# Optimization experiments

Measured on AMD Instinct MI355X. Metric: run time of the kernel, lower is better.

## Reference

```python
import jax, jax.numpy as jnp
import numpy as np

N_HEADS = 16


def setup_inputs() -> dict:
    key = jax.random.key(0)
    ks = jax.random.split(key, 9)
    B, S, D = 2, 2048, 1024
    sc = 0.02
    return {
        'x': jax.random.normal(ks[0], (B, S, D), jnp.float32),
        'Wq': jax.random.normal(ks[1], (D, D), jnp.float32) * sc,
        'bq': jax.random.normal(ks[2], (D,), jnp.float32) * sc,
        'Wk': jax.random.normal(ks[3], (D, D), jnp.float32) * sc,
        'bk': jax.random.normal(ks[4], (D,), jnp.float32) * sc,
        'Wv': jax.random.normal(ks[5], (D, D), jnp.float32) * sc,
        'bv': jax.random.normal(ks[6], (D,), jnp.float32) * sc,
        'Wo': jax.random.normal(ks[7], (D, D), jnp.float32) * sc,
        'bo': jax.random.normal(ks[8], (D,), jnp.float32) * sc,
    }


def reference(x, Wq, bq, Wk, bk, Wv, bv, Wo, bo):
    # Chunked causal prefill. The chunk-wise mask (q_pos >= kv_pos over the
    # growing KV cache) is mathematically identical to full causal attention,
    # so we compute it as one vectorized masked softmax attention.
    B, S, D = x.shape
    H = N_HEADS
    hd = D // H

    def proj(W, b):
        # torch Linear: y = x @ W.T + b ; then split heads -> [B,H,S,hd]
        y = jnp.einsum('bsd,ed->bse', x, W) + b
        return y.reshape(B, S, H, hd).transpose(0, 2, 1, 3)

    q = proj(Wq, bq)
    k = proj(Wk, bk)
    v = proj(Wv, bv)

    scores = jnp.einsum('bhqd,bhkd->bhqk', q, k) / jnp.sqrt(jnp.asarray(hd, x.dtype))
    causal = jnp.tril(jnp.ones((S, S), dtype=bool))  # [S,S]
    scores = jnp.where(causal[None, None], scores, jnp.asarray(-jnp.inf, scores.dtype))
    attn = jax.nn.softmax(scores, axis=-1)
    ctx = jnp.einsum('bhqk,bhkd->bhqd', attn, v)  # [B,H,S,hd]
    ctx = ctx.transpose(0, 2, 1, 3).reshape(B, S, D)
    out = jnp.einsum('bsd,ed->bse', ctx, Wo) + bo
    return out
```

## Files before the change

### kernel.cpp

```cpp
#include <hip/hip_runtime.h>
#include <cstdint>
#include <math.h>

typedef _Float16 f16;
typedef _Float16 f16x2 __attribute__((ext_vector_type(2)));
typedef _Float16 f16x4 __attribute__((ext_vector_type(4)));
typedef _Float16 f16x8 __attribute__((ext_vector_type(8)));
typedef __fp16   h16x2 __attribute__((ext_vector_type(2)));
typedef float    f32x4 __attribute__((ext_vector_type(4)));

__device__ __forceinline__ f32x4 mfma16(f16x8 a, f16x8 b, f32x4 c) {
  return __builtin_amdgcn_mfma_f32_16x16x32_f16(a, b, c, 0, 0, 0);
}
__device__ __forceinline__ void gl2lds16(const f16* g, f16* l) {
  __builtin_amdgcn_global_load_lds((__attribute__((address_space(1))) void*)(g),
                                   (__attribute__((address_space(3))) void*)(l),
                                   16, 0, 0);
}
__device__ __forceinline__ float fexp2(float x) { return __builtin_amdgcn_exp2f(x); }
__device__ __forceinline__ f16x2 pkrtz(float a, float b) {
  h16x2 r = __builtin_amdgcn_cvt_pkrtz(a, b);
  return __builtin_bit_cast(f16x2, r);
}
__device__ __forceinline__ float dot2acc(f16x2 a, f16x2 b, float c) {
#if __has_builtin(__builtin_amdgcn_fdot2)
  return __builtin_amdgcn_fdot2(__builtin_bit_cast(h16x2, a),
                                __builtin_bit_cast(h16x2, b), c, false);
#else
  return c + (float)a[0] * (float)b[0] + (float)a[1] * (float)b[1];
#endif
}

__global__ __launch_bounds__(256) void cvt_kernel(
    const float* __restrict__ x,  const float* __restrict__ wq, const float* __restrict__ wk,
    const float* __restrict__ wv, const float* __restrict__ wo,
    f16* __restrict__ xh, f16* __restrict__ wqkvh, f16* __restrict__ woh)
{
  const int seg = blockIdx.y;
  const float* src; f16* dst; int n;
  if      (seg == 0) { src = x;  dst = xh;              n = 4194304; }
  else if (seg == 1) { src = wq; dst = wqkvh;           n = 1048576; }
  else if (seg == 2) { src = wk; dst = wqkvh + 1048576; n = 1048576; }
  else if (seg == 3) { src = wv; dst = wqkvh + 2097152; n = 1048576; }
  else               { src = wo; dst = woh;             n = 1048576; }
  const int idx = (int)(blockIdx.x * 256 + threadIdx.x) * 8;
  if (idx >= n) return;
  f32x4 a = *(const f32x4*)(src + idx);
  f32x4 b = *(const f32x4*)(src + idx + 4);
  f16x8 h;
  h[0] = (f16)a[0]; h[1] = (f16)a[1]; h[2] = (f16)a[2]; h[3] = (f16)a[3];
  h[4] = (f16)b[0]; h[5] = (f16)b[1]; h[6] = (f16)b[2]; h[7] = (f16)b[3];
  *(f16x8*)(dst + idx) = h;
}

__global__ __launch_bounds__(256) void gemm_qkv(
    const f16* __restrict__ A, const f16* __restrict__ B,
    const float* __restrict__ bias0, const float* __restrict__ bias1, const float* __restrict__ bias2,
    f16* __restrict__ Qp, f16* __restrict__ Kp, f16* __restrict__ Vp)
{
  constexpr int K = 1024;
  __shared__ __align__(16) f16 As[128 * 32];
  __shared__ __align__(16) f16 Bs[128 * 32];
  const int tid  = threadIdx.x;
  const int wave = tid >> 6, lane = tid & 63;
  const int quad = lane >> 4, col = lane & 15;
  const int tile_m = blockIdx.y * 128, tile_n = blockIdx.x * 128;
  const int mb = (wave >> 1) * 64, nb = (wave & 1) * 64;
  const int srow = lane >> 2, scol = (lane & 3) * 8;
  const f16* gA = A + (size_t)(tile_m + wave * 32 + srow) * K + scol;
  const f16* gB = B + (size_t)(tile_n + wave * 32 + srow) * K + scol;
  f16* lA = As + wave * 1024;
  f16* lB = Bs + wave * 1024;

  f32x4 acc[4][4] = {};
  for (int k0 = 0; k0 < K; k0 += 32) {
    gl2lds16(gA + k0,          lA);
    gl2lds16(gA + 16 * K + k0, lA + 512);
    gl2lds16(gB + k0,          lB);
    gl2lds16(gB + 16 * K + k0, lB + 512);
    __syncthreads();
    f16x8 af[4], bf[4];
    #pragma unroll
    for (int i = 0; i < 4; ++i)
      af[i] = *(const f16x8*)&As[(mb + i * 16 + col) * 32 + quad * 8];
    #pragma unroll
    for (int j = 0; j < 4; ++j)
      bf[j] = *(const f16x8*)&Bs[(nb + j * 16 + col) * 32 + quad * 8];
    #pragma unroll
    for (int i = 0; i < 4; ++i)
      #pragma unroll
      for (int j = 0; j < 4; ++j)
        acc[i][j] = mfma16(af[i], bf[j], acc[i][j]);
    __syncthreads();
  }

  #pragma unroll
  for (int j = 0; j < 4; ++j) {
    const int gn = tile_n + nb + j * 16 + col;
    const int which = gn >> 10;
    const int d = gn & 1023;
    const float* bp = (which == 0) ? bias0 : (which == 1) ? bias1 : bias2;
    f16* dst        = (which == 0) ? Qp    : (which == 1) ? Kp    : Vp;
    const float bvv = bp[d];
    const float qs  = (which == 0) ? 0.18033688f : 1.0f;
    const int h = d >> 6, hi = d & 63;
    #pragma unroll
    for (int i = 0; i < 4; ++i) {
      #pragma unroll
      for (int r = 0; r < 4; ++r) {
        const int gm = tile_m + mb + i * 16 + quad * 4 + r;
        const int bb = gm >> 11, s = gm & 2047;
        dst[(((size_t)bb * 16 + h) * 2048 + s) * 64 + hi] = (f16)((acc[i][j][r] + bvv) * qs);
      }
    }
  }
}

__global__ __launch_bounds__(256) void vtrans_kernel(
    const f16* __restrict__ Vh, f16* __restrict__ Vt)
{
  __shared__ __align__(16) f16 t[64][72];
  const int bh = blockIdx.y;
  const int s0 = blockIdx.x * 64;
  const int tid = threadIdx.x;
  const int sr = tid >> 2, dc = (tid & 3) * 16;
  const size_t ib = ((size_t)bh * 2048 + s0 + sr) * 64 + dc;
  f16x8 v0 = *(const f16x8*)&Vh[ib];
  f16x8 v1 = *(const f16x8*)&Vh[ib + 8];
  *(f16x8*)&t[sr][dc]     = v0;
  *(f16x8*)&t[sr][dc + 8] = v1;
  __syncthreads();
  const int d = tid >> 2, sc = (tid & 3) * 16;
  f16x8 o0, o1;
  #pragma unroll
  for (int j = 0; j < 8; ++j) { o0[j] = t[sc + j][d]; o1[j] = t[sc + 8 + j][d]; }
  const size_t ob = ((size_t)bh * 64 + d) * 2048 + s0 + sc;
  *(f16x8*)&Vt[ob]     = o0;
  *(f16x8*)&Vt[ob + 8] = o1;
}

__global__ __launch_bounds__(128) void attn_kernel(
    const f16* __restrict__ Q, const f16* __restrict__ K, const f16* __restrict__ Vt,
    f16* __restrict__ ctx)
{
  __shared__ __align__(16) f16 Ks[64 * 72];
  __shared__ __align__(16) f16 Vts[64 * 72];
  __shared__ __align__(16) f16 Ps[2][32 * 72];
  __shared__ __align__(16) float abuf[2][32];
  __shared__ __align__(16) float lbuf[2][32];

  const int bh  = blockIdx.y;
  const int tid = threadIdx.x;
  const int wave = tid >> 6, lane = tid & 63;
  const int quad = lane >> 4, col = lane & 15;
  const int b = bh >> 4, h = bh & 15;
  const size_t base = (size_t)bh * 2048 * 64;
  const size_t vtb  = (size_t)bh * 64 * 2048;

  int srow[4], sc8[4];
  #pragma unroll
  for (int i = 0; i < 4; ++i) {
    const int flat = tid + i * 128;
    srow[i] = flat >> 3;
    sc8[i]  = (flat & 7) * 8;
  }

  auto run_tile = [&](int qt) {
    const int q0 = qt * 64;
    const int qa = q0 + wave * 16;
    const int qb = q0 + 32 + wave * 16;
    const f16x8 bqa0 = *(const f16x8*)&Q[base + (size_t)(qa + col) * 64 + quad * 8];
    const f16x8 bqa1 = *(const f16x8*)&Q[base + (size_t)(qa + col) * 64 + 32 + quad * 8];
    const f16x8 bqb0 = *(const f16x8*)&Q[base + (size_t)(qb + col) * 64 + quad * 8];
    const f16x8 bqb1 = *(const f16x8*)&Q[base + (size_t)(qb + col) * 64 + 32 + quad * 8];

    f32x4 cta[4] = {}, ctb[4] = {};
    float ma = -INFINITY, la = 0.f, mb = -INFINITY, lb = 0.f;

    f16x8 kr[4], vr[4];
    auto gload = [&](int t) {
      #pragma unroll
      for (int i = 0; i < 4; ++i) {
        kr[i] = *(const f16x8*)&K[base + (size_t)(t * 64 + srow[i]) * 64 + sc8[i]];
        vr[i] = *(const f16x8*)&Vt[vtb + (size_t)srow[i] * 2048 + t * 64 + sc8[i]];
      }
    };
    gload(0);

    const int nIter = qt + 1;
    for (int t = 0; t < nIter; ++t) {
      __syncthreads();
      #pragma unroll
      for (int i = 0; i < 4; ++i) {
        *(f16x8*)&Ks[srow[i] * 72 + sc8[i]]  = kr[i];
        *(f16x8*)&Vts[srow[i] * 72 + sc8[i]] = vr[i];
      }
      __syncthreads();
      if (t + 1 < nIter) gload(t + 1);

      f32x4 sa[4], sb[4];
      #pragma unroll
      for (int jt = 0; jt < 4; ++jt) {
        const int kro = (jt * 16 + col) * 72;
        const f16x8 ak0 = *(const f16x8*)&Ks[kro + quad * 8];
        const f16x8 ak1 = *(const f16x8*)&Ks[kro + 32 + quad * 8];
        f32x4 za = {}, zb = {};
        za = mfma16(ak0, bqa0, za); sa[jt] = mfma16(ak1, bqa1, za);
        zb = mfma16(ak0, bqb0, zb); sb[jt] = mfma16(ak1, bqb1, zb);
      }

      if (t == qt) {
        #pragma unroll
        for (int jt = 0; jt < 4; ++jt) {
          const int kg = t * 64 + jt * 16 + quad * 4;
          #pragma unroll
          for (int r = 0; r < 4; ++r) {
            if (kg + r > qa + col) sa[jt][r] = -1e30f;
            if (kg + r > qb + col) sb[jt][r] = -1e30f;
          }
        }
      }

      const f16x2 one2 = {(_Float16)1.f, (_Float16)1.f};
      {
        float tm = fmaxf(fmaxf(sa[0][0], sa[0][1]), fmaxf(sa[0][2], sa[0][3]));
        #pragma unroll
        for (int jt = 1; jt < 4; ++jt)
          tm = fmaxf(tm, fmaxf(fmaxf(sa[jt][0], sa[jt][1]), fmaxf(sa[jt][2], sa[jt][3])));
        tm = fmaxf(tm, __shfl_xor(tm, 16));
        tm = fmaxf(tm, __shfl_xor(tm, 32));
        const float mnew = fmaxf(ma, tm);
        const float alpha = fexp2(ma - mnew);
        ma = mnew;
        float rs = 0.f;
        #pragma unroll
        for (int jt = 0; jt < 4; ++jt) {
          const f16x2 a01 = pkrtz(fexp2(sa[jt][0] - mnew), fexp2(sa[jt][1] - mnew));
          const f16x2 a23 = pkrtz(fexp2(sa[jt][2] - mnew), fexp2(sa[jt][3] - mnew));
          rs = dot2acc(a01, one2, rs);
          rs = dot2acc(a23, one2, rs);
          f16x4 pw; pw[0] = a01[0]; pw[1] = a01[1]; pw[2] = a23[0]; pw[3] = a23[1];
          *(f16x4*)&Ps[wave][col * 72 + jt * 16 + quad * 4] = pw;
        }
        rs += __shfl_xor(rs, 16);
        rs += __shfl_xor(rs, 32);
        la = la * alpha + rs;
        if (quad == 0) abuf[wave][col] = alpha;
      }
      {
        float tm = fmaxf(fmaxf(sb[0][0], sb[0][1]), fmaxf(sb[0][2], sb[0][3]));
        #pragma unroll
        for (int jt = 1; jt < 4; ++jt)
          tm = fmaxf(tm, fmaxf(fmaxf(sb[jt][0], sb[jt][1]), fmaxf(sb[jt][2], sb[jt][3])));
        tm = fmaxf(tm, __shfl_xor(tm, 16));
        tm = fmaxf(tm, __shfl_xor(tm, 32));
        const float mnew = fmaxf(mb, tm);
        const float alpha = fexp2(mb - mnew);
        mb = mnew;
        float rs = 0.f;
        #pragma unroll
        for (int jt = 0; jt < 4; ++jt) {
          const f16x2 a01 = pkrtz(fexp2(sb[jt][0] - mnew), fexp2(sb[jt][1] - mnew));
          const f16x2 a23 = pkrtz(fexp2(sb[jt][2] - mnew), fexp2(sb[jt][3] - mnew));
          rs = dot2acc(a01, one2, rs);
          rs = dot2acc(a23, one2, rs);
          f16x4 pw; pw[0] = a01[0]; pw[1] = a01[1]; pw[2] = a23[0]; pw[3] = a23[1];
          *(f16x4*)&Ps[wave][(16 + col) * 72 + jt * 16 + quad * 4] = pw;
        }
        rs += __shfl_xor(rs, 16);
        rs += __shfl_xor(rs, 32);
        lb = lb * alpha + rs;
        if (quad == 0) abuf[wave][16 + col] = alpha;
      }

      __asm__ volatile("s_waitcnt lgkmcnt(0)" ::: "memory");
      const f32x4 ava = *(const f32x4*)&abuf[wave][quad * 4];
      const f32x4 avb = *(const f32x4*)&abuf[wave][16 + quad * 4];
      #pragma unroll
      for (int jd = 0; jd < 4; ++jd) { cta[jd] *= ava; ctb[jd] *= avb; }

      const f16x8 apa0 = *(const f16x8*)&Ps[wave][col * 72 + quad * 8];
      const f16x8 apa1 = *(const f16x8*)&Ps[wave][col * 72 + 32 + quad * 8];
      const f16x8 apb0 = *(const f16x8*)&Ps[wave][(16 + col) * 72 + quad * 8];
      const f16x8 apb1 = *(const f16x8*)&Ps[wave][(16 + col) * 72 + 32 + quad * 8];
      #pragma unroll
      for (int jd = 0; jd < 4; ++jd) {
        const int vro = (jd * 16 + col) * 72;
        const f16x8 bv0 = *(const f16x8*)&Vts[vro + quad * 8];
        const f16x8 bv1 = *(const f16x8*)&Vts[vro + 32 + quad * 8];
        cta[jd] = mfma16(apa1, bv1, mfma16(apa0, bv0, cta[jd]));
        ctb[jd] = mfma16(apb1, bv1, mfma16(apb0, bv0, ctb[jd]));
      }
    }

    if (quad == 0) { lbuf[wave][col] = la; lbuf[wave][16 + col] = lb; }
    __asm__ volatile("s_waitcnt lgkmcnt(0)" ::: "memory");
    const f32x4 lva = *(const f32x4*)&lbuf[wave][quad * 4];
    const f32x4 lvb = *(const f32x4*)&lbuf[wave][16 + quad * 4];
    #pragma unroll
    for (int jd = 0; jd < 4; ++jd) {
      #pragma unroll
      for (int r = 0; r < 4; ++r) {
        const int qga = qa + quad * 4 + r;
        const int qgb = qb + quad * 4 + r;
        const int d = h * 64 + jd * 16 + col;
        ctx[((size_t)b * 2048 + qga) * 1024 + d] = (f16)(cta[jd][r] / lva[r]);
        ctx[((size_t)b * 2048 + qgb) * 1024 + d] = (f16)(ctb[jd][r] / lvb[r]);
      }
    }
  };

  run_tile(blockIdx.x);
  run_tile(31 - blockIdx.x);
}

__global__ __launch_bounds__(256) void gemm_o(
    const f16* __restrict__ A, const f16* __restrict__ B, const float* __restrict__ bias,
    float* __restrict__ Out)
{
  constexpr int K = 1024;
  __shared__ __align__(16) f16 As[128 * 32];
  __shared__ __align__(16) f16 Bs[64 * 32];
  const int tid  = threadIdx.x;
  const int wave = tid >> 6, lane = tid & 63;
  const int quad = lane >> 4, col = lane & 15;
  const int tile_m = blockIdx.y * 128, tile_n = blockIdx.x * 64;
  const int mb = wave * 32;
  const int srow = lane >> 2, scol = (lane & 3) * 8;
  const f16* gA = A + (size_t)(tile_m + wave * 32 + srow) * K + scol;
  const f16* gB = B + (size_t)(tile_n + wave * 16 + srow) * K + scol;
  f16* lA = As + wave * 1024;
  f16* lB = Bs + wave * 512;

  f32x4 acc[2][4] = {};
  for (int k0 = 0; k0 < K; k0 += 32) {
    gl2lds16(gA + k0,          lA);
    gl2lds16(gA + 16 * K + k0, lA + 512);
    gl2lds16(gB + k0,          lB);
    __syncthreads();
    f16x8 af[2], bf[4];
    #pragma unroll
    for (int i = 0; i < 2; ++i)
      af[i] = *(const f16x8*)&As[(mb + i * 16 + col) * 32 + quad * 8];
    #pragma unroll
    for (int j = 0; j < 4; ++j)
      bf[j] = *(const f16x8*)&Bs[(j * 16 + col) * 32 + quad * 8];
    #pragma unroll
    for (int i = 0; i < 2; ++i)
      #pragma unroll
      for (int j = 0; j < 4; ++j)
        acc[i][j] = mfma16(af[i], bf[j], acc[i][j]);
    __syncthreads();
  }

  #pragma unroll
  for (int j = 0; j < 4; ++j) {
    const int gn = tile_n + j * 16 + col;
    const float bvv = bias[gn];
    #pragma unroll
    for (int i = 0; i < 2; ++i) {
      #pragma unroll
      for (int r = 0; r < 4; ++r) {
        const int gm = tile_m + mb + i * 16 + quad * 4 + r;
        Out[(size_t)gm * 1024 + gn] = acc[i][j][r] + bvv;
      }
    }
  }
}

extern "C" void kernel_launch(void* const* d_in, const int* in_sizes, int n_in,
                              void* d_out, int out_size, void* d_ws, size_t ws_size,
                              hipStream_t stream)
{
  const float* x  = (const float*)d_in[0];
  const float* Wq = (const float*)d_in[1];
  const float* bq = (const float*)d_in[2];
  const float* Wk = (const float*)d_in[3];
  const float* bk = (const float*)d_in[4];
  const float* Wv = (const float*)d_in[5];
  const float* bv = (const float*)d_in[6];
  const float* Wo = (const float*)d_in[7];
  const float* bo = (const float*)d_in[8];
  float* out = (float*)d_out;

  f16* ws = (f16*)d_ws;
  const size_t M1 = 1048576;
  f16* xh    = ws;
  f16* wqkvh = ws + 4  * M1;
  f16* woh   = ws + 7  * M1;
  f16* Qh    = ws + 8  * M1;
  f16* Kh    = ws + 12 * M1;
  f16* Vh    = ws + 16 * M1;
  f16* Vth   = ws + 20 * M1;
  f16* ctxh  = ws + 24 * M1;

  cvt_kernel<<<dim3(2048, 5), 256, 0, stream>>>(x, Wq, Wk, Wv, Wo, xh, wqkvh, woh);
  gemm_qkv<<<dim3(24, 32), 256, 0, stream>>>(xh, wqkvh, bq, bk, bv, Qh, Kh, Vh);
  vtrans_kernel<<<dim3(32, 32), 256, 0, stream>>>(Vh, Vth);
  attn_kernel<<<dim3(16, 32), 128, 0, stream>>>(Qh, Kh, Vth, ctxh);
  gemm_o<<<dim3(16, 32), 256, 0, stream>>>(ctxh, woh, bo, out);
}
```

Baseline: 202.0 us.

## Fuse V transpose into QKV GEMM epilogue and split attention tiles per block

The QKV GEMM epilogue now writes V straight into the transposed [b,h,d,s] layout using 4-wide f16 stores, so the separate vtrans kernel and its extra Vh buffer go away. The attention kernel launches one q-tile per block (32x32 grid, with heads on x) instead of pairing two tiles per block. This removes a kernel launch and a full read and write of V, and gives more blocks for scheduling. Without the pairing, block work is uneven along the causal length, and the heads-on-x ordering changes which blocks run together and share K/V in cache.

```diff
diff --git a/kernel.cpp b/kernel.cpp
--- a/kernel.cpp
+++ b/kernel.cpp
@@ -56,7 +56,7 @@
 __global__ __launch_bounds__(256) void gemm_qkv(
     const f16* __restrict__ A, const f16* __restrict__ B,
     const float* __restrict__ bias0, const float* __restrict__ bias1, const float* __restrict__ bias2,
-    f16* __restrict__ Qp, f16* __restrict__ Kp, f16* __restrict__ Vp)
+    f16* __restrict__ Qp, f16* __restrict__ Kp, f16* __restrict__ Vtp)
 {
   constexpr int K = 1024;
   __shared__ __align__(16) f16 As[128 * 32];
@@ -99,44 +99,34 @@
     const int gn = tile_n + nb + j * 16 + col;
     const int which = gn >> 10;
     const int d = gn & 1023;
-    const float* bp = (which == 0) ? bias0 : (which == 1) ? bias1 : bias2;
-    f16* dst        = (which == 0) ? Qp    : (which == 1) ? Kp    : Vp;
-    const float bvv = bp[d];
-    const float qs  = (which == 0) ? 0.18033688f : 1.0f;
     const int h = d >> 6, hi = d & 63;
-    #pragma unroll
-    for (int i = 0; i < 4; ++i) {
-      #pragma unroll
-      for (int r = 0; r < 4; ++r) {
-        const int gm = tile_m + mb + i * 16 + quad * 4 + r;
-        const int bb = gm >> 11, s = gm & 2047;
-        dst[(((size_t)bb * 16 + h) * 2048 + s) * 64 + hi] = (f16)((acc[i][j][r] + bvv) * qs);
-      }
-    }
-  }
-}
-
-__global__ __launch_bounds__(256) void vtrans_kernel(
-    const f16* __restrict__ Vh, f16* __restrict__ Vt)
-{
-  __shared__ __align__(16) f16 t[64][72];
-  const int bh = blockIdx.y;
-  const int s0 = blockIdx.x * 64;
-  const int tid = threadIdx.x;
-  const int sr = tid >> 2, dc = (tid & 3) * 16;
-  const size_t ib = ((size_t)bh * 2048 + s0 + sr) * 64 + dc;
-  f16x8 v0 = *(const f16x8*)&Vh[ib];
-  f16x8 v1 = *(const f16x8*)&Vh[ib + 8];
-  *(f16x8*)&t[sr][dc]     = v0;
-  *(f16x8*)&t[sr][dc + 8] = v1;
-  __syncthreads();
-  const int d = tid >> 2, sc = (tid & 3) * 16;
-  f16x8 o0, o1;
-  #pragma unroll
-  for (int j = 0; j < 8; ++j) { o0[j] = t[sc + j][d]; o1[j] = t[sc + 8 + j][d]; }
-  const size_t ob = ((size_t)bh * 64 + d) * 2048 + s0 + sc;
-  *(f16x8*)&Vt[ob]     = o0;
-  *(f16x8*)&Vt[ob + 8] = o1;
+    if (which == 2) {
+      const float bvv = bias2[d];
+      #pragma unroll
+      for (int i = 0; i < 4; ++i) {
+        const int gm0 = tile_m + mb + i * 16 + quad * 4;
+        const int bb = gm0 >> 11, s = gm0 & 2047;
+        f16x4 pw;
+        #pragma unroll
+        for (int r = 0; r < 4; ++r) pw[r] = (f16)(acc[i][j][r] + bvv);
+        *(f16x4*)&Vtp[(((size_t)bb * 16 + h) * 64 + hi) * 2048 + s] = pw;
+      }
+    } else {
+      const float* bp = (which == 0) ? bias0 : bias1;
+      f16* dst        = (which == 0) ? Qp    : Kp;
+      const float bvv = bp[d];
+      const float qs  = (which == 0) ? 0.18033688f : 1.0f;
+      #pragma unroll
+      for (int i = 0; i < 4; ++i) {
+        #pragma unroll
+        for (int r = 0; r < 4; ++r) {
+          const int gm = tile_m + mb + i * 16 + quad * 4 + r;
+          const int bb = gm >> 11, s = gm & 2047;
+          dst[(((size_t)bb * 16 + h) * 2048 + s) * 64 + hi] = (f16)((acc[i][j][r] + bvv) * qs);
+        }
+      }
+    }
+  }
 }
 
 __global__ __launch_bounds__(128) void attn_kernel(
@@ -149,7 +139,9 @@
   __shared__ __align__(16) float abuf[2][32];
   __shared__ __align__(16) float lbuf[2][32];
 
-  const int bh  = blockIdx.y;
+  const int bh  = blockIdx.x;
+  const int by  = blockIdx.y;
+  const int qt  = (by < 16) ? by : 47 - by;
   const int tid = threadIdx.x;
   const int wave = tid >> 6, lane = tid & 63;
   const int quad = lane >> 4, col = lane & 15;
@@ -165,153 +157,148 @@
     sc8[i]  = (flat & 7) * 8;
   }
 
-  auto run_tile = [&](int qt) {
-    const int q0 = qt * 64;
-    const int qa = q0 + wave * 16;
-    const int qb = q0 + 32 + wave * 16;
-    const f16x8 bqa0 = *(const f16x8*)&Q[base + (size_t)(qa + col) * 64 + quad * 8];
-    const f16x8 bqa1 = *(const f16x8*)&Q[base + (size_t)(qa + col) * 64 + 32 + quad * 8];
-    const f16x8 bqb0 = *(const f16x8*)&Q[base + (size_t)(qb + col) * 64 + quad * 8];
-    const f16x8 bqb1 = *(const f16x8*)&Q[base + (size_t)(qb + col) * 64 + 32 + quad * 8];
-
-    f32x4 cta[4] = {}, ctb[4] = {};
-    float ma = -INFINITY, la = 0.f, mb = -INFINITY, lb = 0.f;
-
-    f16x8 kr[4], vr[4];
-    auto gload = [&](int t) {
-      #pragma unroll
-      for (int i = 0; i < 4; ++i) {
-        kr[i] = *(const f16x8*)&K[base + (size_t)(t * 64 + srow[i]) * 64 + sc8[i]];
-        vr[i] = *(const f16x8*)&Vt[vtb + (size_t)srow[i] * 2048 + t * 64 + sc8[i]];
-      }
-    };
-    gload(0);
-
-    const int nIter = qt + 1;
-    for (int t = 0; t < nIter; ++t) {
-      __syncthreads();
-      #pragma unroll
-      for (int i = 0; i < 4; ++i) {
-        *(f16x8*)&Ks[srow[i] * 72 + sc8[i]]  = kr[i];
-        *(f16x8*)&Vts[srow[i] * 72 + sc8[i]] = vr[i];
-      }
-      __syncthreads();
-      if (t + 1 < nIter) gload(t + 1);
-
-      f32x4 sa[4], sb[4];
+  const int q0 = qt * 64;
+  const int qa = q0 + wave * 16;
+  const int qb = q0 + 32 + wave * 16;
+  const f16x8 bqa0 = *(const f16x8*)&Q[base + (size_t)(qa + col) * 64 + quad * 8];
+  const f16x8 bqa1 = *(const f16x8*)&Q[base + (size_t)(qa + col) * 64 + 32 + quad * 8];
+  const f16x8 bqb0 = *(const f16x8*)&Q[base + (size_t)(qb + col) * 64 + quad * 8];
+  const f16x8 bqb1 = *(const f16x8*)&Q[base + (size_t)(qb + col) * 64 + 32 + quad * 8];
+
+  f32x4 cta[4] = {}, ctb[4] = {};
+  float ma = -INFINITY, la = 0.f, mb = -INFINITY, lb = 0.f;
+
+  f16x8 kr[4], vr[4];
+  auto gload = [&](int t) {
+    #pragma unroll
+    for (int i = 0; i < 4; ++i) {
+      kr[i] = *(const f16x8*)&K[base + (size_t)(t * 64 + srow[i]) * 64 + sc8[i]];
+      vr[i] = *(const f16x8*)&Vt[vtb + (size_t)srow[i] * 2048 + t * 64 + sc8[i]];
+    }
+  };
+  gload(0);
+
+  const int nIter = qt + 1;
+  for (int t = 0; t < nIter; ++t) {
+    __syncthreads();
+    #pragma unroll
+    for (int i = 0; i < 4; ++i) {
+      *(f16x8*)&Ks[srow[i] * 72 + sc8[i]]  = kr[i];
+      *(f16x8*)&Vts[srow[i] * 72 + sc8[i]] = vr[i];
+    }
+    __syncthreads();
+    if (t + 1 < nIter) gload(t + 1);
+
+    f32x4 sa[4], sb[4];
+    #pragma unroll
+    for (int jt = 0; jt < 4; ++jt) {
+      const int kro = (jt * 16 + col) * 72;
+      const f16x8 ak0 = *(const f16x8*)&Ks[kro + quad * 8];
+      const f16x8 ak1 = *(const f16x8*)&Ks[kro + 32 + quad * 8];
+      f32x4 za = {}, zb = {};
+      za = mfma16(ak0, bqa0, za); sa[jt] = mfma16(ak1, bqa1, za);
+      zb = mfma16(ak0, bqb0, zb); sb[jt] = mfma16(ak1, bqb1, zb);
+    }
+
+    if (t == qt) {
       #pragma unroll
       for (int jt = 0; jt < 4; ++jt) {
-        const int kro = (jt * 16 + col) * 72;
-        const f16x8 ak0 = *(const f16x8*)&Ks[kro + quad * 8];
-        const f16x8 ak1 = *(const f16x8*)&Ks[kro + 32 + quad * 8];
-        f32x4 za = {}, zb = {};
-        za = mfma16(ak0, bqa0, za); sa[jt] = mfma16(ak1, bqa1, za);
-        zb = mfma16(ak0, bqb0, zb); sb[jt] = mfma16(ak1, bqb1, zb);
-      }
-
-      if (t == qt) {
+        const int kg = t * 64 + jt * 16 + quad * 4;
         #pragma unroll
-        for (int jt = 0; jt < 4; ++jt) {
-          const int kg = t * 64 + jt * 16 + quad * 4;
-          #pragma unroll
-          for (int r = 0; r < 4; ++r) {
-            if (kg + r > qa + col) sa[jt][r] = -1e30f;
-            if (kg + r > qb + col) sb[jt][r] = -1e30f;
-          }
+        for (int r = 0; r < 4; ++r) {
+          if (kg + r > qa + col) sa[jt][r] = -1e30f;
+          if (kg + r > qb + col) sb[jt][r] = -1e30f;
         }
       }
-
-      const f16x2 one2 = {(_Float16)1.f, (_Float16)1.f};
-      {
-        float tm = fmaxf(fmaxf(sa[0][0], sa[0][1]), fmaxf(sa[0][2], sa[0][3]));
-        #pragma unroll
-        for (int jt = 1; jt < 4; ++jt)
-          tm = fmaxf(tm, fmaxf(fmaxf(sa[jt][0], sa[jt][1]), fmaxf(sa[jt][2], sa[jt][3])));
-        tm = fmaxf(tm, __shfl_xor(tm, 16));
-        tm = fmaxf(tm, __shfl_xor(tm, 32));
-        const float mnew = fmaxf(ma, tm);
-        const float alpha = fexp2(ma - mnew);
-        ma = mnew;
-        float rs = 0.f;
-        #pragma unroll
-        for (int jt = 0; jt < 4; ++jt) {
-          const f16x2 a01 = pkrtz(fexp2(sa[jt][0] - mnew), fexp2(sa[jt][1] - mnew));
-          const f16x2 a23 = pkrtz(fexp2(sa[jt][2] - mnew), fexp2(sa[jt][3] - mnew));
-          rs = dot2acc(a01, one2, rs);
-          rs = dot2acc(a23, one2, rs);
-          f16x4 pw; pw[0] = a01[0]; pw[1] = a01[1]; pw[2] = a23[0]; pw[3] = a23[1];
-          *(f16x4*)&Ps[wave][col * 72 + jt * 16 + quad * 4] = pw;
-        }
-        rs += __shfl_xor(rs, 16);
-        rs += __shfl_xor(rs, 32);
-        la = la * alpha + rs;
-        if (quad == 0) abuf[wave][col] = alpha;
-      }
-      {
-        float tm = fmaxf(fmaxf(sb[0][0], sb[0][1]), fmaxf(sb[0][2], sb[0][3]));
-        #pragma unroll
-        for (int jt = 1; jt < 4; ++jt)
-          tm = fmaxf(tm, fmaxf(fmaxf(sb[jt][0], sb[jt][1]), fmaxf(sb[jt][2], sb[jt][3])));
-        tm = fmaxf(tm, __shfl_xor(tm, 16));
-        tm = fmaxf(tm, __shfl_xor(tm, 32));
-        const float mnew = fmaxf(mb, tm);
-        const float alpha = fexp2(mb - mnew);
-        mb = mnew;
-        float rs = 0.f;
-        #pragma unroll
-        for (int jt = 0; jt < 4; ++jt) {
-          const f16x2 a01 = pkrtz(fexp2(sb[jt][0] - mnew), fexp2(sb[jt][1] - mnew));
-          const f16x2 a23 = pkrtz(fexp2(sb[jt][2] - mnew), fexp2(sb[jt][3] - mnew));
-          rs = dot2acc(a01, one2, rs);
-          rs = dot2acc(a23, one2, rs);
-          f16x4 pw; pw[0] = a01[0]; pw[1] = a01[1]; pw[2] = a23[0]; pw[3] = a23[1];
-          *(f16x4*)&Ps[wave][(16 + col) * 72 + jt * 16 + quad * 4] = pw;
-        }
-        rs += __shfl_xor(rs, 16);
-        rs += __shfl_xor(rs, 32);
-        lb = lb * alpha + rs;
-        if (quad == 0) abuf[wave][16 + col] = alpha;
-      }
-
-      __asm__ volatile("s_waitcnt lgkmcnt(0)" ::: "memory");
-      const f32x4 ava = *(const f32x4*)&abuf[wave][quad * 4];
-      const f32x4 avb = *(const f32x4*)&abuf[wave][16 + quad * 4];
-      #pragma unroll
-      for (int jd = 0; jd < 4; ++jd) { cta[jd] *= ava; ctb[jd] *= avb; }
-
-      const f16x8 apa0 = *(const f16x8*)&Ps[wave][col * 72 + quad * 8];
-      const f16x8 apa1 = *(const f16x8*)&Ps[wave][col * 72 + 32 + quad * 8];
-      const f16x8 apb0 = *(const f16x8*)&Ps[wave][(16 + col) * 72 + quad * 8];
-      const f16x8 apb1 = *(const f16x8*)&Ps[wave][(16 + col) * 72 + 32 + quad * 8];
-      #pragma unroll
-      for (int jd = 0; jd < 4; ++jd) {
-        const int vro = (jd * 16 + col) * 72;
-        const f16x8 bv0 = *(const f16x8*)&Vts[vro + quad * 8];
-        const f16x8 bv1 = *(const f16x8*)&Vts[vro + 32 + quad * 8];
-        cta[jd] = mfma16(apa1, bv1, mfma16(apa0, bv0, cta[jd]));
-        ctb[jd] = mfma16(apb1, bv1, mfma16(apb0, bv0, ctb[jd]));
-      }
-    }
-
-    if (quad == 0) { lbuf[wave][col] = la; lbuf[wave][16 + col] = lb; }
+    }
+
+    const f16x2 one2 = {(_Float16)1.f, (_Float16)1.f};
+    {
+      float tm = fmaxf(fmaxf(sa[0][0], sa[0][1]), fmaxf(sa[0][2], sa[0][3]));
+      #pragma unroll
+      for (int jt = 1; jt < 4; ++jt)
+        tm = fmaxf(tm, fmaxf(fmaxf(sa[jt][0], sa[jt][1]), fmaxf(sa[jt][2], sa[jt][3])));
+      tm = fmaxf(tm, __shfl_xor(tm, 16));
+      tm = fmaxf(tm, __shfl_xor(tm, 32));
+      const float mnew = fmaxf(ma, tm);
+      const float alpha = fexp2(ma - mnew);
+      ma = mnew;
+      float rs = 0.f;
+      #pragma unroll
+      for (int jt = 0; jt < 4; ++jt) {
+        const f16x2 a01 = pkrtz(fexp2(sa[jt][0] - mnew), fexp2(sa[jt][1] - mnew));
+        const f16x2 a23 = pkrtz(fexp2(sa[jt][2] - mnew), fexp2(sa[jt][3] - mnew));
+        rs = dot2acc(a01, one2, rs);
+        rs = dot2acc(a23, one2, rs);
+        f16x4 pw; pw[0] = a01[0]; pw[1] = a01[1]; pw[2] = a23[0]; pw[3] = a23[1];
+        *(f16x4*)&Ps[wave][col * 72 + jt * 16 + quad * 4] = pw;
+      }
+      rs += __shfl_xor(rs, 16);
+      rs += __shfl_xor(rs, 32);
+      la = la * alpha + rs;
+      if (quad == 0) abuf[wave][col] = alpha;
+    }
+    {
+      float tm = fmaxf(fmaxf(sb[0][0], sb[0][1]), fmaxf(sb[0][2], sb[0][3]));
+      #pragma unroll
+      for (int jt = 1; jt < 4; ++jt)
+        tm = fmaxf(tm, fmaxf(fmaxf(sb[jt][0], sb[jt][1]), fmaxf(sb[jt][2], sb[jt][3])));
+      tm = fmaxf(tm, __shfl_xor(tm, 16));
+      tm = fmaxf(tm, __shfl_xor(tm, 32));
+      const float mnew = fmaxf(mb, tm);
+      const float alpha = fexp2(mb - mnew);
+      mb = mnew;
+      float rs = 0.f;
+      #pragma unroll
+      for (int jt = 0; jt < 4; ++jt) {
+        const f16x2 a01 = pkrtz(fexp2(sb[jt][0] - mnew), fexp2(sb[jt][1] - mnew));
+        const f16x2 a23 = pkrtz(fexp2(sb[jt][2] - mnew), fexp2(sb[jt][3] - mnew));
+        rs = dot2acc(a01, one2, rs);
+        rs = dot2acc(a23, one2, rs);
+        f16x4 pw; pw[0] = a01[0]; pw[1] = a01[1]; pw[2] = a23[0]; pw[3] = a23[1];
+        *(f16x4*)&Ps[wave][(16 + col) * 72 + jt * 16 + quad * 4] = pw;
+      }
+      rs += __shfl_xor(rs, 16);
+      rs += __shfl_xor(rs, 32);
+      lb = lb * alpha + rs;
+      if (quad == 0) abuf[wave][16 + col] = alpha;
+    }
+
     __asm__ volatile("s_waitcnt lgkmcnt(0)" ::: "memory");
-    const f32x4 lva = *(const f32x4*)&lbuf[wave][quad * 4];
-    const f32x4 lvb = *(const f32x4*)&lbuf[wave][16 + quad * 4];
+    const f32x4 ava = *(const f32x4*)&abuf[wave][quad * 4];
+    const f32x4 avb = *(const f32x4*)&abuf[wave][16 + quad * 4];
+    #pragma unroll
+    for (int jd = 0; jd < 4; ++jd) { cta[jd] *= ava; ctb[jd] *= avb; }
+
+    const f16x8 apa0 = *(const f16x8*)&Ps[wave][col * 72 + quad * 8];
+    const f16x8 apa1 = *(const f16x8*)&Ps[wave][col * 72 + 32 + quad * 8];
+    const f16x8 apb0 = *(const f16x8*)&Ps[wave][(16 + col) * 72 + quad * 8];
+    const f16x8 apb1 = *(const f16x8*)&Ps[wave][(16 + col) * 72 + 32 + quad * 8];
     #pragma unroll
     for (int jd = 0; jd < 4; ++jd) {
-      #pragma unroll
-      for (int r = 0; r < 4; ++r) {
-        const int qga = qa + quad * 4 + r;
-        const int qgb = qb + quad * 4 + r;
-        const int d = h * 64 + jd * 16 + col;
-        ctx[((size_t)b * 2048 + qga) * 1024 + d] = (f16)(cta[jd][r] / lva[r]);
-        ctx[((size_t)b * 2048 + qgb) * 1024 + d] = (f16)(ctb[jd][r] / lvb[r]);
-      }
-    }
-  };
-
-  run_tile(blockIdx.x);
-  run_tile(31 - blockIdx.x);
+      const int vro = (jd * 16 + col) * 72;
+      const f16x8 bv0 = *(const f16x8*)&Vts[vro + quad * 8];
+      const f16x8 bv1 = *(const f16x8*)&Vts[vro + 32 + quad * 8];
+      cta[jd] = mfma16(apa1, bv1, mfma16(apa0, bv0, cta[jd]));
+      ctb[jd] = mfma16(apb1, bv1, mfma16(apb0, bv0, ctb[jd]));
+    }
+  }
+
+  if (quad == 0) { lbuf[wave][col] = la; lbuf[wave][16 + col] = lb; }
+  __asm__ volatile("s_waitcnt lgkmcnt(0)" ::: "memory");
+  const f32x4 lva = *(const f32x4*)&lbuf[wave][quad * 4];
+  const f32x4 lvb = *(const f32x4*)&lbuf[wave][16 + quad * 4];
+  #pragma unroll
+  for (int jd = 0; jd < 4; ++jd) {
+    #pragma unroll
+    for (int r = 0; r < 4; ++r) {
+      const int qga = qa + quad * 4 + r;
+      const int qgb = qb + quad * 4 + r;
+      const int d = h * 64 + jd * 16 + col;
+      ctx[((size_t)b * 2048 + qga) * 1024 + d] = (f16)(cta[jd][r] / lva[r]);
+      ctx[((size_t)b * 2048 + qgb) * 1024 + d] = (f16)(ctb[jd][r] / lvb[r]);
+    }
+  }
 }
 
 __global__ __launch_bounds__(256) void gemm_o(
@@ -390,13 +377,11 @@
   f16* woh   = ws + 7  * M1;
   f16* Qh    = ws + 8  * M1;
   f16* Kh    = ws + 12 * M1;
-  f16* Vh    = ws + 16 * M1;
-  f16* Vth   = ws + 20 * M1;
-  f16* ctxh  = ws + 24 * M1;
+  f16* Vth   = ws + 16 * M1;
+  f16* ctxh  = ws + 20 * M1;
 
   cvt_kernel<<<dim3(2048, 5), 256, 0, stream>>>(x, Wq, Wk, Wv, Wo, xh, wqkvh, woh);
-  gemm_qkv<<<dim3(24, 32), 256, 0, stream>>>(xh, wqkvh, bq, bk, bv, Qh, Kh, Vh);
-  vtrans_kernel<<<dim3(32, 32), 256, 0, stream>>>(Vh, Vth);
-  attn_kernel<<<dim3(16, 32), 128, 0, stream>>>(Qh, Kh, Vth, ctxh);
+  gemm_qkv<<<dim3(24, 32), 256, 0, stream>>>(xh, wqkvh, bq, bk, bv, Qh, Kh, Vth);
+  attn_kernel<<<dim3(32, 32), 128, 0, stream>>>(Qh, Kh, Vth, ctxh);
   gemm_o<<<dim3(16, 32), 256, 0, stream>>>(ctxh, woh, bo, out);
 }
```

New measurement: 214.2 us. 6.0% more time.
